# Performance work log

Hardware: AMD Instinct MI355X
Metric: run time of the kernel (lower is better)

The kernel has to match this reference:

```python
import jax, jax.numpy as jnp
import numpy as np

D_MODEL = 1024
NUM_HEAD = 16
BATCH = 2
SEQ = 2048
NEG_INF = -1e9  # matches masked_fill value in the original


def setup_inputs() -> dict:
    key = jax.random.key(0)
    k1, k2, k3, k4, k5 = jax.random.split(key, 5)
    scale = 1.0 / np.sqrt(D_MODEL)
    return {
        "x": jax.random.normal(k1, (BATCH, SEQ, D_MODEL), dtype=jnp.float32),
        "q_weight": jax.random.normal(k2, (D_MODEL, D_MODEL), dtype=jnp.float32) * scale,
        "k_weight": jax.random.normal(k3, (D_MODEL, D_MODEL), dtype=jnp.float32) * scale,
        "v_weight": jax.random.normal(k4, (D_MODEL, D_MODEL), dtype=jnp.float32) * scale,
        "o_weight": jax.random.normal(k5, (D_MODEL, D_MODEL), dtype=jnp.float32) * scale,
    }


def reference(x, q_weight, k_weight, v_weight, o_weight):
    b, s, d = x.shape
    h = NUM_HEAD
    dh = d // h
    # projections: weight layout is (d_out, d_in)
    q = jnp.einsum('bsd,ed->bse', x, q_weight).reshape(b, s, h, dh).transpose(0, 2, 1, 3)
    k = jnp.einsum('bsd,ed->bse', x, k_weight).reshape(b, s, h, dh).transpose(0, 2, 1, 3)
    v = jnp.einsum('bsd,ed->bse', x, v_weight).reshape(b, s, h, dh).transpose(0, 2, 1, 3)
    scores = jnp.einsum('bhqd,bhkd->bhqk', q, k) / jnp.sqrt(jnp.asarray(dh, x.dtype))
    causal = jnp.triu(jnp.ones((s, s), dtype=bool), k=1)  # True above diagonal -> masked
    scores = jnp.where(causal, jnp.asarray(NEG_INF, x.dtype), scores)
    attn = jax.nn.softmax(scores, axis=-1)
    out = jnp.einsum('bhqk,bhkd->bhqd', attn, v)          # [b,h,s,dh]
    out = out.transpose(0, 2, 1, 3).reshape(b, s, d)       # merge heads
    return jnp.einsum('bse,de->bsd', out, o_weight)
```

## Files before the change

### kernel.cpp

```cpp
#include <hip/hip_runtime.h>

typedef short bhalf8 __attribute__((ext_vector_type(8)));
typedef float floatx4 __attribute__((ext_vector_type(4)));

#define D_MODEL 1024
#define SEQ     2048
#define BATCH   2
#define NHEAD   16
#define DH      64

#define GLDS(g, l) __builtin_amdgcn_global_load_lds( \
    (const __attribute__((address_space(1))) void*)(g), \
    (__attribute__((address_space(3))) void*)(l), 16, 0, 0)

static __device__ __forceinline__ short f2bf(float f) {
    unsigned u = __builtin_bit_cast(unsigned, f);
    u = (u + 0x7fffu + ((u >> 16) & 1u)) >> 16;
    return (short)u;
}
static __device__ __forceinline__ unsigned pack2(float a, float b) {
    return (unsigned)(unsigned short)f2bf(a) | ((unsigned)(unsigned short)f2bf(b) << 16);
}

__global__ __launch_bounds__(256) void cast_x(const float* __restrict__ s,
                                              short* __restrict__ d) {
    int i = (blockIdx.x * 256 + threadIdx.x) * 8;
    float4 a = *(const float4*)(s + i);
    float4 b = *(const float4*)(s + i + 4);
    uint4 u = {pack2(a.x, a.y), pack2(a.z, a.w), pack2(b.x, b.y), pack2(b.z, b.w)};
    *(uint4*)(d + i) = u;
}

__global__ __launch_bounds__(256) void cast_w(const float* __restrict__ wq,
                                              const float* __restrict__ wk,
                                              const float* __restrict__ wv,
                                              const float* __restrict__ wo,
                                              short* __restrict__ dst) {
    const float* s = (blockIdx.y == 0) ? wq : (blockIdx.y == 1) ? wk
                   : (blockIdx.y == 2) ? wv : wo;
    size_t off = (size_t)blockIdx.y * (D_MODEL * D_MODEL);
    int i = (blockIdx.x * 256 + threadIdx.x) * 8;
    float4 a = *(const float4*)(s + i);
    float4 b = *(const float4*)(s + i + 4);
    uint4 u = {pack2(a.x, a.y), pack2(a.z, a.w), pack2(b.x, b.y), pack2(b.z, b.w)};
    *(uint4*)(dst + off + i) = u;
}

__global__ __launch_bounds__(256) void gemm_qkv(const short* __restrict__ A,
                                                const short* __restrict__ W,
                                                short* __restrict__ Qo,
                                                short* __restrict__ Ko,
                                                short* __restrict__ Vt) {
    __shared__ __align__(16) char pool[34816];
    short (*As)[64] = (short(*)[64])pool;
    short (*Bs)[64] = (short(*)[64])(pool + 16384);
    const int t    = threadIdx.x;
    const int wave = t >> 6, lane = t & 63, quad = lane >> 4, l16 = lane & 15;
    const int bm = blockIdx.x * 128, by = blockIdx.y, bn = by * 128;
    const int qm = (wave >> 1) * 64, qn = (wave & 1) * 64;

    const int lrow = lane >> 3, lcol = (lane & 7) * 8;
    const short* Ag = A + (size_t)(bm + wave * 32 + lrow) * 1024 + lcol;
    const short* Wg = W + (size_t)(bn + wave * 32 + lrow) * 1024 + lcol;
    short* Al = &As[wave * 32][0];
    short* Bl = &Bs[wave * 32][0];

    floatx4 acc[4][4];
#pragma unroll
    for (int i = 0; i < 4; ++i)
#pragma unroll
        for (int j = 0; j < 4; ++j) {
            floatx4 z = {0.f, 0.f, 0.f, 0.f};
            acc[i][j] = z;
        }

    for (int k0 = 0; k0 < 1024; k0 += 64) {
        __syncthreads();
#pragma unroll
        for (int j = 0; j < 4; ++j) {
            GLDS(Ag + k0 + (size_t)j * 8 * 1024, Al + j * 8 * 64);
            GLDS(Wg + k0 + (size_t)j * 8 * 1024, Bl + j * 8 * 64);
        }
        __syncthreads();
#pragma unroll
        for (int kk = 0; kk < 64; kk += 32) {
            bhalf8 af[4], bfr[4];
#pragma unroll
            for (int im = 0; im < 4; ++im)
                af[im] = *(const bhalf8*)&As[qm + im * 16 + l16][kk + quad * 8];
#pragma unroll
            for (int jn = 0; jn < 4; ++jn)
                bfr[jn] = *(const bhalf8*)&Bs[qn + jn * 16 + l16][kk + quad * 8];
#pragma unroll
            for (int im = 0; im < 4; ++im)
#pragma unroll
                for (int jn = 0; jn < 4; ++jn)
                    acc[im][jn] = __builtin_amdgcn_mfma_f32_16x16x32_bf16(
                        af[im], bfr[jn], acc[im][jn], 0, 0, 0);
        }
    }

    __syncthreads();
    short (*Ct)[136] = (short(*)[136])pool;
    const bool isV = (by >= 16);
#pragma unroll
    for (int im = 0; im < 4; ++im)
#pragma unroll
        for (int jn = 0; jn < 4; ++jn)
#pragma unroll
            for (int g = 0; g < 4; ++g) {
                const int ml = qm + im * 16 + quad * 4 + g;
                const int nl = qn + jn * 16 + l16;
                if (isV) Ct[nl][ml] = f2bf(acc[im][jn][g]);
                else     Ct[ml][nl] = f2bf(acc[im][jn][g]);
            }
    __syncthreads();

    short* outp;
    size_t rowbase, colbase, stride;
    if (by < 8)       { outp = Qo; rowbase = bm;                colbase = bn;        stride = 1024; }
    else if (by < 16) { outp = Ko; rowbase = bm;                colbase = bn - 1024; stride = 1024; }
    else              { outp = Vt; rowbase = (size_t)bn - 2048; colbase = bm;        stride = 4096; }
#pragma unroll
    for (int pass = 0; pass < 8; ++pass) {
        const int r = (t >> 4) + pass * 16;
        const int c = (t & 15) * 8;
        uint4 u = *(const uint4*)&Ct[r][c];
        *(uint4*)(outp + (rowbase + r) * stride + colbase + c) = u;
    }
}

__global__ __launch_bounds__(256) void gemm_o(const short* __restrict__ A,
                                              const short* __restrict__ W,
                                              float* __restrict__ C) {
    __shared__ __align__(16) char pool[34816];
    short (*As)[64] = (short(*)[64])pool;
    short (*Bs)[64] = (short(*)[64])(pool + 16384);
    const int t    = threadIdx.x;
    const int wave = t >> 6, lane = t & 63, quad = lane >> 4, l16 = lane & 15;
    const int bm = blockIdx.x * 128, bn = blockIdx.y * 64;
    const int qm = (wave >> 1) * 64, qn = (wave & 1) * 32;

    const int lrow = lane >> 3, lcol = (lane & 7) * 8;
    const short* Ag = A + (size_t)(bm + wave * 32 + lrow) * 1024 + lcol;
    const short* Wg = W + (size_t)(bn + wave * 16 + lrow) * 1024 + lcol;
    short* Al = &As[wave * 32][0];
    short* Bl = &Bs[wave * 16][0];

    floatx4 acc[4][2];
#pragma unroll
    for (int i = 0; i < 4; ++i)
#pragma unroll
        for (int j = 0; j < 2; ++j) {
            floatx4 z = {0.f, 0.f, 0.f, 0.f};
            acc[i][j] = z;
        }

    for (int k0 = 0; k0 < 1024; k0 += 64) {
        __syncthreads();
#pragma unroll
        for (int j = 0; j < 4; ++j)
            GLDS(Ag + k0 + (size_t)j * 8 * 1024, Al + j * 8 * 64);
#pragma unroll
        for (int j = 0; j < 2; ++j)
            GLDS(Wg + k0 + (size_t)j * 8 * 1024, Bl + j * 8 * 64);
        __syncthreads();
#pragma unroll
        for (int kk = 0; kk < 64; kk += 32) {
            bhalf8 af[4], bfr[2];
#pragma unroll
            for (int im = 0; im < 4; ++im)
                af[im] = *(const bhalf8*)&As[qm + im * 16 + l16][kk + quad * 8];
#pragma unroll
            for (int jn = 0; jn < 2; ++jn)
                bfr[jn] = *(const bhalf8*)&Bs[qn + jn * 16 + l16][kk + quad * 8];
#pragma unroll
            for (int im = 0; im < 4; ++im)
#pragma unroll
                for (int jn = 0; jn < 2; ++jn)
                    acc[im][jn] = __builtin_amdgcn_mfma_f32_16x16x32_bf16(
                        af[im], bfr[jn], acc[im][jn], 0, 0, 0);
        }
    }

    __syncthreads();
    float (*Ctf)[68] = (float(*)[68])pool;
#pragma unroll
    for (int im = 0; im < 4; ++im)
#pragma unroll
        for (int jn = 0; jn < 2; ++jn)
#pragma unroll
            for (int g = 0; g < 4; ++g)
                Ctf[qm + im * 16 + quad * 4 + g][qn + jn * 16 + l16] = acc[im][jn][g];
    __syncthreads();
#pragma unroll
    for (int pass = 0; pass < 8; ++pass) {
        const int r = (t >> 4) + pass * 16;
        const int c = (t & 15) * 4;
        float4 u = *(const float4*)&Ctf[r][c];
        *(float4*)(C + (size_t)(bm + r) * 1024 + bn + c) = u;
    }
}

__global__ __launch_bounds__(256) void attn_v4(const short* __restrict__ Qo,
                                               const short* __restrict__ Ko,
                                               const short* __restrict__ Vt,
                                               short* __restrict__ Y) {
    __shared__ __align__(16) char pool[34816];
    short (*Ks)[64] = (short(*)[64])pool;
    short (*Vs)[64] = (short(*)[64])(pool + 8192);
    short (*Ps)[72] = (short(*)[72])(pool + 16384);
    const int t    = threadIdx.x;
    const int wave = t >> 6, lane = t & 63, quad = lane >> 4, l16 = lane & 15;
    const int bh = blockIdx.x, b = bh >> 4, h = bh & 15;
    const int qb = (int)(gridDim.y - 1 - blockIdx.y) * 128;
    const int qw = qb + wave * 32;

    const short* Qbase = Qo + (size_t)b * SEQ * 1024 + h * 64;
    const short* Kbase = Ko + (size_t)b * SEQ * 1024 + h * 64;
    const short* Vbase = Vt + (size_t)h * 64 * 4096 + (size_t)b * SEQ;

    bhalf8 qf[2][2];
#pragma unroll
    for (int im = 0; im < 2; ++im) {
        const short* qr = Qbase + (size_t)(qw + im * 16 + l16) * 1024;
        qf[im][0] = *(const bhalf8*)(qr + quad * 8);
        qf[im][1] = *(const bhalf8*)(qr + 32 + quad * 8);
    }

    float lsum[2][4];
    floatx4 o[2][4];
#pragma unroll
    for (int im = 0; im < 2; ++im)
#pragma unroll
        for (int g = 0; g < 4; ++g) lsum[im][g] = 0.f;
#pragma unroll
    for (int im = 0; im < 2; ++im)
#pragma unroll
        for (int nd = 0; nd < 4; ++nd) {
            floatx4 z = {0.f, 0.f, 0.f, 0.f};
            o[im][nd] = z;
        }

    const float KS = 0.125f * 1.44269504f;
    const float CB = 12.0f * 1.44269504f;

    const int lrow = lane >> 3, lcol = (lane & 7) * 8;
    const short* Kg = Kbase + (size_t)(wave * 16 + lrow) * 1024 + lcol;
    const short* Vg = Vbase + (size_t)(wave * 16 + lrow) * 4096 + lcol;
    short* Kl = &Ks[wave * 16][0];
    short* Vl = &Vs[wave * 16][0];

    const int nchunks = qb / 64 + 2;
    for (int ic = 0; ic < nchunks; ++ic) {
        const int k0 = ic * 64;
        __syncthreads();
#pragma unroll
        for (int j = 0; j < 2; ++j) {
            GLDS(Kg + (size_t)(k0 + j * 8) * 1024, Kl + j * 8 * 64);
            GLDS(Vg + (size_t)j * 8 * 4096 + k0,   Vl + j * 8 * 64);
        }
        __syncthreads();

        if (k0 < qw + 32) {
            bhalf8 kf[4][2];
#pragma unroll
            for (int jn = 0; jn < 4; ++jn) {
                kf[jn][0] = *(const bhalf8*)&Ks[jn * 16 + l16][quad * 8];
                kf[jn][1] = *(const bhalf8*)&Ks[jn * 16 + l16][32 + quad * 8];
            }
            floatx4 s[2][4];
#pragma unroll
            for (int im = 0; im < 2; ++im)
#pragma unroll
                for (int jn = 0; jn < 4; ++jn) {
                    floatx4 z = {0.f, 0.f, 0.f, 0.f};
                    z = __builtin_amdgcn_mfma_f32_16x16x32_bf16(qf[im][0], kf[jn][0], z, 0, 0, 0);
                    z = __builtin_amdgcn_mfma_f32_16x16x32_bf16(qf[im][1], kf[jn][1], z, 0, 0, 0);
                    s[im][jn] = z;
                }

            const bool partial = (k0 + 64 > qw);
#pragma unroll
            for (int im = 0; im < 2; ++im)
#pragma unroll
                for (int g = 0; g < 4; ++g) {
                    const int rr = im * 16 + quad * 4 + g;
                    const int qrow = qw + rr;
                    float e0 = exp2f(s[im][0][g] * KS - CB);
                    float e1 = exp2f(s[im][1][g] * KS - CB);
                    float e2 = exp2f(s[im][2][g] * KS - CB);
                    float e3 = exp2f(s[im][3][g] * KS - CB);
                    if (partial) {
                        if (k0 + l16 > qrow)      e0 = 0.f;
                        if (k0 + 16 + l16 > qrow) e1 = 0.f;
                        if (k0 + 32 + l16 > qrow) e2 = 0.f;
                        if (k0 + 48 + l16 > qrow) e3 = 0.f;
                    }
                    lsum[im][g] += (e0 + e1) + (e2 + e3);
                    Ps[wave * 32 + rr][l16]      = f2bf(e0);
                    Ps[wave * 32 + rr][16 + l16] = f2bf(e1);
                    Ps[wave * 32 + rr][32 + l16] = f2bf(e2);
                    Ps[wave * 32 + rr][48 + l16] = f2bf(e3);
                }

            bhalf8 vt[4][2];
#pragma unroll
            for (int nd = 0; nd < 4; ++nd) {
                vt[nd][0] = *(const bhalf8*)&Vs[nd * 16 + l16][quad * 8];
                vt[nd][1] = *(const bhalf8*)&Vs[nd * 16 + l16][32 + quad * 8];
            }
#pragma unroll
            for (int im = 0; im < 2; ++im) {
                bhalf8 ap0 = *(const bhalf8*)&Ps[wave * 32 + im * 16 + l16][quad * 8];
                bhalf8 ap1 = *(const bhalf8*)&Ps[wave * 32 + im * 16 + l16][32 + quad * 8];
#pragma unroll
                for (int nd = 0; nd < 4; ++nd) {
                    o[im][nd] = __builtin_amdgcn_mfma_f32_16x16x32_bf16(ap0, vt[nd][0], o[im][nd], 0, 0, 0);
                    o[im][nd] = __builtin_amdgcn_mfma_f32_16x16x32_bf16(ap1, vt[nd][1], o[im][nd], 0, 0, 0);
                }
            }
        }
    }

    float inv[2][4];
#pragma unroll
    for (int im = 0; im < 2; ++im)
#pragma unroll
        for (int g = 0; g < 4; ++g) {
            float r = lsum[im][g];
            r += __shfl_xor(r, 1, 64);
            r += __shfl_xor(r, 2, 64);
            r += __shfl_xor(r, 4, 64);
            r += __shfl_xor(r, 8, 64);
            inv[im][g] = 1.0f / r;
        }
#pragma unroll
    for (int im = 0; im < 2; ++im)
#pragma unroll
        for (int nd = 0; nd < 4; ++nd)
#pragma unroll
            for (int g = 0; g < 4; ++g) {
                const int qrow = qw + im * 16 + quad * 4 + g;
                Y[(size_t)(b * SEQ + qrow) * 1024 + h * 64 + nd * 16 + l16] =
                    f2bf(o[im][nd][g] * inv[im][g]);
            }
}

extern "C" void kernel_launch(void* const* d_in, const int* in_sizes, int n_in,
                              void* d_out, int out_size, void* d_ws, size_t ws_size,
                              hipStream_t stream) {
    const float* x  = (const float*)d_in[0];
    const float* wq = (const float*)d_in[1];
    const float* wk = (const float*)d_in[2];
    const float* wv = (const float*)d_in[3];
    const float* wo = (const float*)d_in[4];

    short* xb   = (short*)d_ws;
    short* Qo   = xb + (size_t)4096 * 1024;
    short* Ko   = Qo + (size_t)4096 * 1024;
    short* Vt   = Ko + (size_t)4096 * 1024;
    short* wall = Vt + (size_t)1024 * 4096;
    short* wob  = wall + (size_t)3 * 1024 * 1024;

    cast_x<<<dim3(2048), 256, 0, stream>>>(x, xb);
    cast_w<<<dim3(512, 4), 256, 0, stream>>>(wq, wk, wv, wo, wall);
    gemm_qkv<<<dim3(32, 24), 256, 0, stream>>>(xb, wall, Qo, Ko, Vt);
    attn_v4<<<dim3(BATCH * NHEAD, SEQ / 128), 256, 0, stream>>>(Qo, Ko, Vt, xb);
    gemm_o<<<dim3(32, 16), 256, 0, stream>>>(xb, wob, (float*)d_out);
}
```

Before: 227.5 us.

## Load K/V tiles directly from global into registers per wave, drop shared staging

The attention kernel no longer stages K and V chunks cooperatively in LDS behind block-wide barriers. Each wave now reads its K and V MFMA fragments straight from global memory and iterates only over the key range its own rows need. Only the per-wave P buffer stays in shared memory. This removes both __syncthreads per chunk and the idle chunks that waves past the diagonal used to sit through, at the cost of each wave issuing its own redundant, less coalesced global loads that must now be served by cache.

```diff
diff --git a/kernel.cpp b/kernel.cpp
--- a/kernel.cpp
+++ b/kernel.cpp
@@ -202,14 +202,11 @@
     }
 }
 
-__global__ __launch_bounds__(256) void attn_v4(const short* __restrict__ Qo,
+__global__ __launch_bounds__(256) void attn_v5(const short* __restrict__ Qo,
                                                const short* __restrict__ Ko,
                                                const short* __restrict__ Vt,
                                                short* __restrict__ Y) {
-    __shared__ __align__(16) char pool[34816];
-    short (*Ks)[64] = (short(*)[64])pool;
-    short (*Vs)[64] = (short(*)[64])(pool + 8192);
-    short (*Ps)[72] = (short(*)[72])(pool + 16384);
+    __shared__ __align__(16) short Ps[4][32][72];
     const int t    = threadIdx.x;
     const int wave = t >> 6, lane = t & 63, quad = lane >> 4, l16 = lane & 15;
     const int bh = blockIdx.x, b = bh >> 4, h = bh & 15;
@@ -245,80 +242,65 @@
     const float KS = 0.125f * 1.44269504f;
     const float CB = 12.0f * 1.44269504f;
 
-    const int lrow = lane >> 3, lcol = (lane & 7) * 8;
-    const short* Kg = Kbase + (size_t)(wave * 16 + lrow) * 1024 + lcol;
-    const short* Vg = Vbase + (size_t)(wave * 16 + lrow) * 4096 + lcol;
-    short* Kl = &Ks[wave * 16][0];
-    short* Vl = &Vs[wave * 16][0];
-
-    const int nchunks = qb / 64 + 2;
-    for (int ic = 0; ic < nchunks; ++ic) {
-        const int k0 = ic * 64;
-        __syncthreads();
-#pragma unroll
-        for (int j = 0; j < 2; ++j) {
-            GLDS(Kg + (size_t)(k0 + j * 8) * 1024, Kl + j * 8 * 64);
-            GLDS(Vg + (size_t)j * 8 * 4096 + k0,   Vl + j * 8 * 64);
-        }
-        __syncthreads();
-
-        if (k0 < qw + 32) {
-            bhalf8 kf[4][2];
+    for (int k0 = 0; k0 < qw + 32; k0 += 64) {
+        bhalf8 kf[4][2];
+#pragma unroll
+        for (int jn = 0; jn < 4; ++jn) {
+            const short* kr = Kbase + (size_t)(k0 + jn * 16 + l16) * 1024 + quad * 8;
+            kf[jn][0] = *(const bhalf8*)(kr);
+            kf[jn][1] = *(const bhalf8*)(kr + 32);
+        }
+        bhalf8 vt[4][2];
+#pragma unroll
+        for (int nd = 0; nd < 4; ++nd) {
+            const short* vr = Vbase + (size_t)(nd * 16 + l16) * 4096 + k0 + quad * 8;
+            vt[nd][0] = *(const bhalf8*)(vr);
+            vt[nd][1] = *(const bhalf8*)(vr + 32);
+        }
+
+        floatx4 s[2][4];
+#pragma unroll
+        for (int im = 0; im < 2; ++im)
 #pragma unroll
             for (int jn = 0; jn < 4; ++jn) {
-                kf[jn][0] = *(const bhalf8*)&Ks[jn * 16 + l16][quad * 8];
-                kf[jn][1] = *(const bhalf8*)&Ks[jn * 16 + l16][32 + quad * 8];
-            }
-            floatx4 s[2][4];
-#pragma unroll
-            for (int im = 0; im < 2; ++im)
-#pragma unroll
-                for (int jn = 0; jn < 4; ++jn) {
-                    floatx4 z = {0.f, 0.f, 0.f, 0.f};
-                    z = __builtin_amdgcn_mfma_f32_16x16x32_bf16(qf[im][0], kf[jn][0], z, 0, 0, 0);
-                    z = __builtin_amdgcn_mfma_f32_16x16x32_bf16(qf[im][1], kf[jn][1], z, 0, 0, 0);
-                    s[im][jn] = z;
+                floatx4 z = {0.f, 0.f, 0.f, 0.f};
+                z = __builtin_amdgcn_mfma_f32_16x16x32_bf16(qf[im][0], kf[jn][0], z, 0, 0, 0);
+                z = __builtin_amdgcn_mfma_f32_16x16x32_bf16(qf[im][1], kf[jn][1], z, 0, 0, 0);
+                s[im][jn] = z;
+            }
+
+        const bool partial = (k0 + 64 > qw);
+#pragma unroll
+        for (int im = 0; im < 2; ++im)
+#pragma unroll
+            for (int g = 0; g < 4; ++g) {
+                const int rr = im * 16 + quad * 4 + g;
+                const int qrow = qw + rr;
+                float e0 = exp2f(s[im][0][g] * KS - CB);
+                float e1 = exp2f(s[im][1][g] * KS - CB);
+                float e2 = exp2f(s[im][2][g] * KS - CB);
+                float e3 = exp2f(s[im][3][g] * KS - CB);
+                if (partial) {
+                    if (k0 + l16 > qrow)      e0 = 0.f;
+                    if (k0 + 16 + l16 > qrow) e1 = 0.f;
+                    if (k0 + 32 + l16 > qrow) e2 = 0.f;
+                    if (k0 + 48 + l16 > qrow) e3 = 0.f;
                 }
-
-            const bool partial = (k0 + 64 > qw);
-#pragma unroll
-            for (int im = 0; im < 2; ++im)
-#pragma unroll
-                for (int g = 0; g < 4; ++g) {
-                    const int rr = im * 16 + quad * 4 + g;
-                    const int qrow = qw + rr;
-                    float e0 = exp2f(s[im][0][g] * KS - CB);
-                    float e1 = exp2f(s[im][1][g] * KS - CB);
-                    float e2 = exp2f(s[im][2][g] * KS - CB);
-                    float e3 = exp2f(s[im][3][g] * KS - CB);
-                    if (partial) {
-                        if (k0 + l16 > qrow)      e0 = 0.f;
-                        if (k0 + 16 + l16 > qrow) e1 = 0.f;
-                        if (k0 + 32 + l16 > qrow) e2 = 0.f;
-                        if (k0 + 48 + l16 > qrow) e3 = 0.f;
-                    }
-                    lsum[im][g] += (e0 + e1) + (e2 + e3);
-                    Ps[wave * 32 + rr][l16]      = f2bf(e0);
-                    Ps[wave * 32 + rr][16 + l16] = f2bf(e1);
-                    Ps[wave * 32 + rr][32 + l16] = f2bf(e2);
-                    Ps[wave * 32 + rr][48 + l16] = f2bf(e3);
-                }
-
-            bhalf8 vt[4][2];
+                lsum[im][g] += (e0 + e1) + (e2 + e3);
+                Ps[wave][rr][l16]      = f2bf(e0);
+                Ps[wave][rr][16 + l16] = f2bf(e1);
+                Ps[wave][rr][32 + l16] = f2bf(e2);
+                Ps[wave][rr][48 + l16] = f2bf(e3);
+            }
+
+#pragma unroll
+        for (int im = 0; im < 2; ++im) {
+            bhalf8 ap0 = *(const bhalf8*)&Ps[wave][im * 16 + l16][quad * 8];
+            bhalf8 ap1 = *(const bhalf8*)&Ps[wave][im * 16 + l16][32 + quad * 8];
 #pragma unroll
             for (int nd = 0; nd < 4; ++nd) {
-                vt[nd][0] = *(const bhalf8*)&Vs[nd * 16 + l16][quad * 8];
-                vt[nd][1] = *(const bhalf8*)&Vs[nd * 16 + l16][32 + quad * 8];
-            }
-#pragma unroll
-            for (int im = 0; im < 2; ++im) {
-                bhalf8 ap0 = *(const bhalf8*)&Ps[wave * 32 + im * 16 + l16][quad * 8];
-                bhalf8 ap1 = *(const bhalf8*)&Ps[wave * 32 + im * 16 + l16][32 + quad * 8];
-#pragma unroll
-                for (int nd = 0; nd < 4; ++nd) {
-                    o[im][nd] = __builtin_amdgcn_mfma_f32_16x16x32_bf16(ap0, vt[nd][0], o[im][nd], 0, 0, 0);
-                    o[im][nd] = __builtin_amdgcn_mfma_f32_16x16x32_bf16(ap1, vt[nd][1], o[im][nd], 0, 0, 0);
-                }
+                o[im][nd] = __builtin_amdgcn_mfma_f32_16x16x32_bf16(ap0, vt[nd][0], o[im][nd], 0, 0, 0);
+                o[im][nd] = __builtin_amdgcn_mfma_f32_16x16x32_bf16(ap1, vt[nd][1], o[im][nd], 0, 0, 0);
             }
         }
     }
@@ -366,6 +348,6 @@
     cast_x<<<dim3(2048), 256, 0, stream>>>(x, xb);
     cast_w<<<dim3(512, 4), 256, 0, stream>>>(wq, wk, wv, wo, wall);
     gemm_qkv<<<dim3(32, 24), 256, 0, stream>>>(xb, wall, Qo, Ko, Vt);
-    attn_v4<<<dim3(BATCH * NHEAD, SEQ / 128), 256, 0, stream>>>(Qo, Ko, Vt, xb);
+    attn_v5<<<dim3(BATCH * NHEAD, SEQ / 128), 256, 0, stream>>>(Qo, Ko, Vt, xb);
     gemm_o<<<dim3(32, 16), 256, 0, stream>>>(xb, wob, (float*)d_out);
 }
```

New measurement: 241.7 us. 6.3% more time.
